# Optimization experiments

Measured on AMD Instinct MI355X. Metric: run time of the kernel, lower is better.

Reference implementation:

```python
import jax, jax.numpy as jnp
import numpy as np

N, E, F, EF, D, G = 25000, 100000, 32, 8, 64, 1000


def setup_inputs() -> dict:
    key = jax.random.key(0)
    ks = jax.random.split(key, 32)
    p = lambda k, shape: (jax.random.normal(k, shape, jnp.float32) * 0.05)
    inp = {
        "x": jax.random.normal(ks[0], (N, F), jnp.float32),
        "edge_index": jax.random.randint(ks[1], (2, E), 0, N, jnp.int64 if jax.config.jax_enable_x64 else jnp.int32),
        "edge_attr": jax.random.uniform(ks[2], (E, EF), jnp.float32),
        "batch": jnp.sort(jax.random.randint(ks[3], (N,), 0, G, jnp.int32)),
        # lin0
        "W0": p(ks[4], (F, D)), "b0": p(ks[5], (D,)),
        # edge MLP: Linear(EF, D) -> ReLU -> Linear(D, D*D)
        "We1": p(ks[6], (EF, D)), "be1": p(ks[7], (D,)),
        "We2": p(ks[8], (D, D * D)), "be2": p(ks[9], (D * D,)),
        # NNConv root weight + bias
        "Wroot": p(ks[10], (D, D)), "bconv": p(ks[11], (D,)),
        # GRU (single layer): gate order r, z, n
        "Wi": p(ks[12], (3 * D, D)), "Wh": p(ks[13], (3 * D, D)),
        "bi": p(ks[14], (3 * D,)), "bh": p(ks[15], (3 * D,)),
        # heads
        "W11": p(ks[16], (D, D)), "b11": p(ks[17], (D,)),
        "W12": p(ks[18], (D, D)), "b12": p(ks[19], (D,)),
        "W13": p(ks[20], (D, 1)), "b13": p(ks[21], (1,)),
        "W21": p(ks[22], (D, D)), "b21": p(ks[23], (D,)),
        "W22": p(ks[24], (D, D)), "b22": p(ks[25], (D,)),
        "W23": p(ks[26], (D, 1)), "b23": p(ks[27], (1,)),
    }
    return inp


def reference(x, edge_index, edge_attr, batch,
              W0, b0, We1, be1, We2, be2, Wroot, bconv,
              Wi, Wh, bi, bh,
              W11, b11, W12, b12, W13, b13,
              W21, b21, W22, b22, W23, b23):
    src, dst = edge_index[0], edge_index[1]
    # lin0 + relu
    x1 = jax.nn.relu(x @ W0 + b0)                      # [N, D]
    h = x1                                              # GRU hidden init
    # NNConv: dynamic per-edge weight via edge MLP
    ew = (jax.nn.relu(edge_attr @ We1 + be1) @ We2 + be2).reshape(E, D, D)
    msg = jnp.einsum('ei,eio->eo', x1[src], ew)        # per-edge matmul
    agg = jax.ops.segment_sum(msg, dst, num_segments=N)
    x2 = jax.nn.relu(x1 @ Wroot + agg + bconv)         # [N, D]
    # GRU single step (torch gate order: r, z, n)
    gi = x2 @ Wi.T + bi
    gh = h @ Wh.T + bh
    r = jax.nn.sigmoid(gi[:, :D] + gh[:, :D])
    z = jax.nn.sigmoid(gi[:, D:2 * D] + gh[:, D:2 * D])
    n = jnp.tanh(gi[:, 2 * D:] + r * gh[:, 2 * D:])
    hn = (1.0 - z) * n + z * h                          # [N, D]
    # graph pooling (scatter_add over batch)
    pooled = jax.ops.segment_sum(hn, batch, num_segments=G)  # [G, D]
    # two MLP heads
    x_1 = jax.nn.relu(pooled @ W11 + b11)
    x_1 = jax.nn.relu(x_1 @ W12 + b12)
    x_1 = x_1 @ W13 + b13
    x_2 = jax.nn.relu(pooled @ W21 + b21)
    x_2 = jax.nn.relu(x_2 @ W22 + b22)
    x_2 = x_2 @ W23 + b23
    return jnp.concatenate([x_1, x_2], axis=1)          # [G, 2]
```

## Files before the change

kernel.cpp:

```cpp
#include <hip/hip_runtime.h>
#include <hip/hip_bf16.h>
#include <hip/hip_fp16.h>

#define NN 25000
#define NE 100000
#define FIN 32
#define DD 64
#define NG 1000

typedef unsigned short u16;
typedef __attribute__((ext_vector_type(8))) short short8;
typedef __attribute__((ext_vector_type(8))) _Float16 f16x8;
typedef __attribute__((ext_vector_type(4))) float f32x4;

__device__ __forceinline__ u16 f2h(float f) {
    __half h = __float2half(f);
    return __builtin_bit_cast(u16, h);
}
__device__ __forceinline__ float h2f(u16 u) {
    __half h = __builtin_bit_cast(__half, u);
    return __half2float(h);
}
__device__ __forceinline__ f16x8 s2h(short8 v) { return __builtin_bit_cast(f16x8, v); }
__device__ __forceinline__ bool idx_is_i64(const int* e) {
    return (e[1] == 0) & (e[3] == 0) & (e[5] == 0) & (e[7] == 0) & (e[9] == 0);
}
__device__ __forceinline__ int ld_src(const int* e, int i, bool i64) {
    return i64 ? e[2 * i] : e[i];
}
__device__ __forceinline__ int ld_dst(const int* e, int i, bool i64) {
    return i64 ? e[2 * (NE + i)] : e[NE + i];
}

__global__ __launch_bounds__(256) void k_pre(const float* __restrict__ x,
                                             const float* __restrict__ W0,
                                             const float* __restrict__ b0,
                                             u16* __restrict__ x1b,
                                             const float* __restrict__ We2,
                                             const float* __restrict__ be2,
                                             float* __restrict__ agg,
                                             float* __restrict__ pooled,
                                             u16* __restrict__ Bt2,
                                             const float* __restrict__ Wi,
                                             const float* __restrict__ Wh,
                                             const float* __restrict__ Wroot,
                                             u16* __restrict__ Wib,
                                             u16* __restrict__ Whb,
                                             u16* __restrict__ Wrb) {
    __shared__ float sbuf[4096 + 512];
    int tid = threadIdx.x;
    if (blockIdx.x < 1563) {
        float* sW = sbuf;
        float* sx = sbuf + 4096;
        for (int i = tid; i < FIN * DD; i += 256) sW[i] = W0[i];
        int nbase = blockIdx.x * 16;
        for (int i = tid; i < 16 * FIN; i += 256) {
            int nl = i >> 5, f = i & 31;
            int n = nbase + nl;
            sx[i] = (n < NN) ? x[n * FIN + f] : 0.f;
        }
        __syncthreads();
        int lane = tid & 63, nl = tid >> 6;
        float bias = b0[lane];
        #pragma unroll
        for (int rr = 0; rr < 4; rr++) {
            int row = nl * 4 + rr;
            int n = nbase + row;
            if (n < NN) {
                float acc = bias;
                #pragma unroll
                for (int f = 0; f < FIN; f++) acc += sx[row * FIN + f] * sW[f * DD + lane];
                x1b[n * DD + lane] = f2h(fmaxf(acc, 0.f));
            }
        }
    } else if (blockIdx.x < 1628) {
        int kc = blockIdx.x - 1563;
        const float* src = (kc < 64) ? (We2 + kc * 4096) : be2;
        for (int i = tid; i < 4096; i += 256) sbuf[i] = src[i];
        __syncthreads();
        for (int m = tid; m < 4096; m += 256) {
            int f = m >> 9, ln = (m >> 3) & 63, j = m & 7;
            int s = f >> 2, c = f & 3;
            int o = c * 16 + (ln & 15);
            int rlow = s * 32 + (ln >> 4) * 8 + j;
            Bt2[kc * 4096 + m] = f2h(sbuf[rlow * 64 + o]);
        }
    } else {
        int tid0 = (blockIdx.x - 1628) * 256 + threadIdx.x;
        const int STR = 256 * 256;
        for (int i = tid0; i < NN * DD; i += STR) agg[i] = 0.f;
        for (int i = tid0; i < NG * DD; i += STR) pooled[i] = 0.f;
        for (int i = tid0; i < 12288; i += STR) {
            int fr = i >> 9, lane = (i >> 3) & 63, j = i & 7;
            int c = fr >> 1, kcx = fr & 1;
            int row = c * 16 + (lane & 15);
            int col = kcx * 32 + (lane >> 4) * 8 + j;
            Wib[i] = f2h(Wi[row * 64 + col]);
            Whb[i] = f2h(Wh[row * 64 + col]);
        }
        for (int i = tid0; i < 4096; i += STR) {
            int fr = i >> 9, lane = (i >> 3) & 63, j = i & 7;
            int c = fr >> 1, kcx = fr & 1;
            int row = c * 16 + (lane & 15);
            int col = kcx * 32 + (lane >> 4) * 8 + j;
            Wrb[i] = f2h(Wroot[col * 64 + row]);
        }
    }
}

__global__ __launch_bounds__(512, 4) void k_msg(const float* __restrict__ ea,
                                                const int* __restrict__ eidx,
                                                const float* __restrict__ We1,
                                                const float* __restrict__ be1,
                                                const u16* __restrict__ x1b,
                                                const u16* __restrict__ Bt2,
                                                float* __restrict__ agg) {
    __shared__ __align__(16) u16 sX[128 * 72];
    __shared__ __align__(16) u16 sTh[65 * 128 + 64];
    __shared__ float sWe1[8 * 64];
    __shared__ float sbe1[64];
    __shared__ int sDst[128];
    const int tid = threadIdx.x;
    const int lane = tid & 63, wv = tid >> 6;
    const int ll = lane & 15, quad = lane >> 4;
    const int rh = wv >> 2, cq = wv & 3;
    const int e0 = blockIdx.x * 128;
    const bool i64 = idx_is_i64(eidx);

    if (tid < 512) sWe1[tid] = We1[tid];
    if (tid < 64) sbe1[tid] = be1[tid];
    if (tid < 128) {
        sDst[tid] = (e0 + tid < NE) ? ld_dst(eidx, e0 + tid, i64) : 0;
        sTh[64 * 128 + tid] = 0x3C00;
    }

    const int el4 = tid >> 2, seg = tid & 3;
    const int eg4 = e0 + el4;
    {
        if (eg4 < NE) {
            int sv = ld_src(eidx, eg4, i64);
            const u16* xr = x1b + sv * 64 + seg * 16;
            *(uint4*)&sX[el4 * 72 + seg * 16]     = *(const uint4*)(xr);
            *(uint4*)&sX[el4 * 72 + seg * 16 + 8] = *(const uint4*)(xr + 8);
        } else {
            uint4 z = make_uint4(0, 0, 0, 0);
            *(uint4*)&sX[el4 * 72 + seg * 16]     = z;
            *(uint4*)&sX[el4 * 72 + seg * 16 + 8] = z;
        }
    }
    float eav[8];
    if (eg4 < NE) {
        f32x4 v0 = *(const f32x4*)(ea + eg4 * 8);
        f32x4 v1 = *(const f32x4*)(ea + eg4 * 8 + 4);
        #pragma unroll
        for (int f = 0; f < 4; f++) { eav[f] = v0[f]; eav[4 + f] = v1[f]; }
    } else {
        #pragma unroll
        for (int f = 0; f < 8; f++) eav[f] = 0.f;
    }
    __syncthreads();

    {
        int k0 = seg * 16;
        for (int kk = 0; kk < 16; kk++) {
            int k = k0 + kk;
            float acc = sbe1[k];
            #pragma unroll
            for (int f = 0; f < 8; f++) acc += eav[f] * sWe1[f * 64 + k];
            sTh[k * 128 + el4] = f2h((eg4 < NE) ? fmaxf(acc, 0.f) : 0.f);
        }
    }
    __syncthreads();

    short8 xa[4][2];
    #pragma unroll
    for (int rt = 0; rt < 4; rt++)
        #pragma unroll
        for (int s = 0; s < 2; s++)
            xa[rt][s] = *(const short8*)&sX[(rh * 64 + rt * 16 + ll) * 72 + s * 32 + quad * 8];

    f32x4 msg[4];
    #pragma unroll
    for (int rt = 0; rt < 4; rt++) msg[rt] = (f32x4){0.f, 0.f, 0.f, 0.f};

    const u16* gB0 = Bt2 + (0 * 4 + cq) * 512 + lane * 8;
    const u16* gB1 = Bt2 + (1 * 4 + cq) * 512 + lane * 8;
    const f32x4 zero = (f32x4){0.f, 0.f, 0.f, 0.f};
    const int tkoff = rh * 64 + quad * 4;

    #define LDR(dst, kcv, rtv) dst = *(const uint2*)&sTh[(kcv) * 128 + tkoff + (rtv) * 16];
    #define CVT(t, raw)                                                      \
        {                                                                    \
            __half2 _a = __builtin_bit_cast(__half2, (raw).x);               \
            __half2 _b = __builtin_bit_cast(__half2, (raw).y);               \
            float2 _fa = __half22float2(_a);                                 \
            float2 _fb = __half22float2(_b);                                 \
            t = (f32x4){_fa.x, _fa.y, _fb.x, _fb.y};                         \
        }

    short8 c00 = *(const short8*)(gB0);
    short8 c01 = *(const short8*)(gB1);
    short8 c10 = *(const short8*)(gB0 + 4096);
    short8 c11 = *(const short8*)(gB1 + 4096);
    uint2 tkA[4], tkB[4];
    #pragma unroll
    for (int rt = 0; rt < 4; rt++) LDR(tkA[rt], 0, rt);

    for (int kc = 0; kc < 62; kc += 2) {
        short8 n00 = *(const short8*)(gB0 + (kc + 2) * 4096);
        short8 n01 = *(const short8*)(gB1 + (kc + 2) * 4096);
        short8 n10 = *(const short8*)(gB0 + (kc + 3) * 4096);
        short8 n11 = *(const short8*)(gB1 + (kc + 3) * 4096);
        #pragma unroll
        for (int rt = 0; rt < 4; rt++) LDR(tkB[rt], kc + 1, rt);
        #pragma unroll
        for (int rt = 0; rt < 4; rt++) {
            f32x4 q0 = __builtin_amdgcn_mfma_f32_16x16x32_f16(s2h(xa[rt][0]), s2h(c00), zero, 0, 0, 0);
            f32x4 q1 = __builtin_amdgcn_mfma_f32_16x16x32_f16(s2h(xa[rt][1]), s2h(c01), zero, 0, 0, 0);
            f32x4 t; CVT(t, tkA[rt]);
            msg[rt] += t * q0;
            msg[rt] += t * q1;
        }
        #pragma unroll
        for (int rt = 0; rt < 4; rt++) LDR(tkA[rt], kc + 2, rt);
        #pragma unroll
        for (int rt = 0; rt < 4; rt++) {
            f32x4 q0 = __builtin_amdgcn_mfma_f32_16x16x32_f16(s2h(xa[rt][0]), s2h(c10), zero, 0, 0, 0);
            f32x4 q1 = __builtin_amdgcn_mfma_f32_16x16x32_f16(s2h(xa[rt][1]), s2h(c11), zero, 0, 0, 0);
            f32x4 t; CVT(t, tkB[rt]);
            msg[rt] += t * q0;
            msg[rt] += t * q1;
        }
        c00 = n00; c01 = n01; c10 = n10; c11 = n11;
    }
    {
        short8 n00 = *(const short8*)(gB0 + 64 * 4096);
        short8 n01 = *(const short8*)(gB1 + 64 * 4096);
        #pragma unroll
        for (int rt = 0; rt < 4; rt++) LDR(tkB[rt], 63, rt);
        #pragma unroll
        for (int rt = 0; rt < 4; rt++) {
            f32x4 q0 = __builtin_amdgcn_mfma_f32_16x16x32_f16(s2h(xa[rt][0]), s2h(c00), zero, 0, 0, 0);
            f32x4 q1 = __builtin_amdgcn_mfma_f32_16x16x32_f16(s2h(xa[rt][1]), s2h(c01), zero, 0, 0, 0);
            f32x4 t; CVT(t, tkA[rt]);
            msg[rt] += t * q0;
            msg[rt] += t * q1;
        }
        #pragma unroll
        for (int rt = 0; rt < 4; rt++) LDR(tkA[rt], 64, rt);
        #pragma unroll
        for (int rt = 0; rt < 4; rt++) {
            f32x4 q0 = __builtin_amdgcn_mfma_f32_16x16x32_f16(s2h(xa[rt][0]), s2h(c10), zero, 0, 0, 0);
            f32x4 q1 = __builtin_amdgcn_mfma_f32_16x16x32_f16(s2h(xa[rt][1]), s2h(c11), zero, 0, 0, 0);
            f32x4 t; CVT(t, tkB[rt]);
            msg[rt] += t * q0;
            msg[rt] += t * q1;
        }
        #pragma unroll
        for (int rt = 0; rt < 4; rt++) {
            f32x4 q0 = __builtin_amdgcn_mfma_f32_16x16x32_f16(s2h(xa[rt][0]), s2h(n00), zero, 0, 0, 0);
            f32x4 q1 = __builtin_amdgcn_mfma_f32_16x16x32_f16(s2h(xa[rt][1]), s2h(n01), zero, 0, 0, 0);
            f32x4 t; CVT(t, tkA[rt]);
            msg[rt] += t * q0;
            msg[rt] += t * q1;
        }
    }
    #undef LDR
    #undef CVT

    #pragma unroll
    for (int rt = 0; rt < 4; rt++) {
        #pragma unroll
        for (int r = 0; r < 4; r++) {
            int el = rh * 64 + rt * 16 + quad * 4 + r;
            int eg = e0 + el;
            if (eg < NE) {
                int d = sDst[el];
                atomicAdd(&agg[d * 64 + cq * 16 + ll], msg[rt][r]);
            }
        }
    }
}

__global__ __launch_bounds__(256) void k_gru(const u16* __restrict__ x1b,
                                             const float* __restrict__ agg,
                                             const u16* __restrict__ Wib,
                                             const u16* __restrict__ Whb,
                                             const u16* __restrict__ Wrb,
                                             const float* __restrict__ bconv,
                                             const float* __restrict__ bi,
                                             const float* __restrict__ bh,
                                             const int* __restrict__ batch,
                                             float* __restrict__ pooled) {
    __shared__ __align__(16) u16 sX2[64 * 72];
    __shared__ float hbuf[64 * 65];
    __shared__ int sBatch[64];
    const int tid = threadIdx.x;
    const int lane = tid & 63, wv = tid >> 6;
    const int ll = lane & 15, quad = lane >> 4;
    const int n0 = blockIdx.x * 64;

    if (tid < 64) {
        int n = n0 + tid;
        sBatch[tid] = (n < NN) ? batch[n] : -1;
    }

    short8 ha[2];
    {
        int n = n0 + wv * 16 + ll;
        #pragma unroll
        for (int kc = 0; kc < 2; kc++) {
            if (n < NN) ha[kc] = *(const short8*)(x1b + n * 64 + kc * 32 + quad * 8);
            else        ha[kc] = (short8){0,0,0,0,0,0,0,0};
        }
    }
    f32x4 acc1[4];
    #pragma unroll
    for (int c = 0; c < 4; c++) acc1[c] = (f32x4){0.f, 0.f, 0.f, 0.f};
    #pragma unroll
    for (int kc = 0; kc < 2; kc++) {
        #pragma unroll
        for (int c = 0; c < 4; c++) {
            short8 b = *(const short8*)&Wrb[(c * 2 + kc) * 512 + lane * 8];
            acc1[c] = __builtin_amdgcn_mfma_f32_16x16x32_f16(s2h(ha[kc]), s2h(b), acc1[c], 0, 0, 0);
        }
    }
    #pragma unroll
    for (int c = 0; c < 4; c++) {
        int col = c * 16 + ll;
        float bcv = bconv[col];
        #pragma unroll
        for (int r = 0; r < 4; r++) {
            int row = wv * 16 + quad * 4 + r;
            int n = n0 + row;
            float v = 0.f;
            if (n < NN) v = fmaxf(acc1[c][r] + agg[n * 64 + col] + bcv, 0.f);
            sX2[row * 72 + col] = f2h(v);
        }
    }
    __syncthreads();

    short8 xa[2];
    #pragma unroll
    for (int kc = 0; kc < 2; kc++)
        xa[kc] = *(const short8*)&sX2[(wv * 16 + ll) * 72 + kc * 32 + quad * 8];

    f32x4 agi[12], agh[12];
    #pragma unroll
    for (int c = 0; c < 12; c++) { agi[c] = (f32x4){0.f,0.f,0.f,0.f}; agh[c] = (f32x4){0.f,0.f,0.f,0.f}; }
    #pragma unroll
    for (int kc = 0; kc < 2; kc++) {
        #pragma unroll
        for (int c = 0; c < 12; c++) {
            short8 bi8 = *(const short8*)&Wib[(c * 2 + kc) * 512 + lane * 8];
            short8 bh8 = *(const short8*)&Whb[(c * 2 + kc) * 512 + lane * 8];
            agi[c] = __builtin_amdgcn_mfma_f32_16x16x32_f16(s2h(xa[kc]), s2h(bi8), agi[c], 0, 0, 0);
            agh[c] = __builtin_amdgcn_mfma_f32_16x16x32_f16(s2h(ha[kc]), s2h(bh8), agh[c], 0, 0, 0);
        }
    }

    float hnv[4][4];
    #pragma unroll
    for (int c0 = 0; c0 < 4; c0++) {
        int d = c0 * 16 + ll;
        float bir = bi[d],        bhr = bh[d];
        float biz = bi[64 + d],   bhz = bh[64 + d];
        float bin = bi[128 + d],  bhn = bh[128 + d];
        #pragma unroll
        for (int r = 0; r < 4; r++) {
            int row = wv * 16 + quad * 4 + r;
            int n = n0 + row;
            float gir = agi[c0][r] + bir,     ghr = agh[c0][r] + bhr;
            float giz = agi[c0 + 4][r] + biz, ghz = agh[c0 + 4][r] + bhz;
            float gin = agi[c0 + 8][r] + bin, ghn = agh[c0 + 8][r] + bhn;
            float rg = 1.f / (1.f + __expf(-(gir + ghr)));
            float zg = 1.f / (1.f + __expf(-(giz + ghz)));
            float ng = tanhf(gin + rg * ghn);
            float hv = (n < NN) ? h2f(x1b[n * 64 + d]) : 0.f;
            hnv[c0][r] = (n < NN) ? ((1.f - zg) * ng + zg * hv) : 0.f;
        }
    }
    __syncthreads();

    #pragma unroll
    for (int c0 = 0; c0 < 4; c0++) {
        int d = c0 * 16 + ll;
        #pragma unroll
        for (int r = 0; r < 4; r++) {
            int row = wv * 16 + quad * 4 + r;
            hbuf[row * 65 + d] = hnv[c0][r];
        }
    }
    __syncthreads();

    {
        int d = lane;
        float sum = 0.f;
        int pb = sBatch[wv * 16];
        #pragma unroll
        for (int rr = 0; rr < 16; rr++) {
            int row = wv * 16 + rr;
            int b = sBatch[row];
            float v = hbuf[row * 65 + d];
            if (b != pb) {
                if (pb >= 0) atomicAdd(&pooled[pb * 64 + d], sum);
                sum = v; pb = b;
            } else {
                sum += v;
            }
        }
        if (pb >= 0) atomicAdd(&pooled[pb * 64 + d], sum);
    }
}

__global__ __launch_bounds__(256) void k_heads(const float* __restrict__ pooled,
                                               const float* __restrict__ W11, const float* __restrict__ b11,
                                               const float* __restrict__ W12, const float* __restrict__ b12,
                                               const float* __restrict__ W13, const float* __restrict__ b13,
                                               const float* __restrict__ W21, const float* __restrict__ b21,
                                               const float* __restrict__ W22, const float* __restrict__ b22,
                                               const float* __restrict__ W23, const float* __restrict__ b23,
                                               float* __restrict__ out) {
    __shared__ float sV[4][64];
    __shared__ float sA[4][64];
    int tid = threadIdx.x, lane = tid & 63, wv = tid >> 6;
    int g = blockIdx.x * 4 + wv;
    if (g >= NG) return;
    float p = pooled[g * 64 + lane];
    sV[wv][lane] = p;
    float y[2];
    const float* W1s[2] = {W11, W21}; const float* b1s[2] = {b11, b21};
    const float* W2s[2] = {W12, W22}; const float* b2s[2] = {b12, b22};
    const float* W3s[2] = {W13, W23}; const float* b3s[2] = {b13, b23};
    #pragma unroll
    for (int hd = 0; hd < 2; hd++) {
        float a = b1s[hd][lane];
        #pragma unroll 8
        for (int i = 0; i < 64; i++) a += sV[wv][i] * W1s[hd][i * 64 + lane];
        a = fmaxf(a, 0.f);
        sA[wv][lane] = a;
        float a2 = b2s[hd][lane];
        #pragma unroll 8
        for (int i = 0; i < 64; i++) a2 += sA[wv][i] * W2s[hd][i * 64 + lane];
        a2 = fmaxf(a2, 0.f);
        float part = a2 * W3s[hd][lane];
        #pragma unroll
        for (int m = 32; m > 0; m >>= 1) part += __shfl_xor(part, m, 64);
        y[hd] = part + b3s[hd][0];
    }
    if (lane == 0) {
        out[g * 2 + 0] = y[0];
        out[g * 2 + 1] = y[1];
    }
}

extern "C" void kernel_launch(void* const* d_in, const int* in_sizes, int n_in,
                              void* d_out, int out_size, void* d_ws, size_t ws_size,
                              hipStream_t stream) {
    const float* x     = (const float*)d_in[0];
    const int* eidx    = (const int*)d_in[1];
    const float* ea    = (const float*)d_in[2];
    const int* batch   = (const int*)d_in[3];
    const float* W0    = (const float*)d_in[4];  const float* b0    = (const float*)d_in[5];
    const float* We1   = (const float*)d_in[6];  const float* be1   = (const float*)d_in[7];
    const float* We2   = (const float*)d_in[8];  const float* be2   = (const float*)d_in[9];
    const float* Wroot = (const float*)d_in[10]; const float* bconv = (const float*)d_in[11];
    const float* Wi    = (const float*)d_in[12]; const float* Wh    = (const float*)d_in[13];
    const float* bi    = (const float*)d_in[14]; const float* bh    = (const float*)d_in[15];
    const float* W11   = (const float*)d_in[16]; const float* b11   = (const float*)d_in[17];
    const float* W12   = (const float*)d_in[18]; const float* b12   = (const float*)d_in[19];
    const float* W13   = (const float*)d_in[20]; const float* b13   = (const float*)d_in[21];
    const float* W21   = (const float*)d_in[22]; const float* b21   = (const float*)d_in[23];
    const float* W22   = (const float*)d_in[24]; const float* b22   = (const float*)d_in[25];
    const float* W23   = (const float*)d_in[26]; const float* b23   = (const float*)d_in[27];
    float* out = (float*)d_out;

    char* ws = (char*)d_ws;
    float* agg    = (float*)(ws);
    u16*   x1b    = (u16*)(ws + 6400000);
    u16*   Bt2    = (u16*)(ws + 9600000);
    float* pooled = (float*)(ws + 10132480);
    u16*   Wib    = (u16*)(ws + 10388480);
    u16*   Whb    = (u16*)(ws + 10413056);
    u16*   Wrb    = (u16*)(ws + 10437632);

    hipLaunchKernelGGL(k_pre, dim3(1884), dim3(256), 0, stream,
                       x, W0, b0, x1b, We2, be2, agg, pooled, Bt2,
                       Wi, Wh, Wroot, Wib, Whb, Wrb);
    hipLaunchKernelGGL(k_msg, dim3(782), dim3(512), 0, stream, ea, eidx, We1, be1, x1b, Bt2, agg);
    hipLaunchKernelGGL(k_gru, dim3(391), dim3(256), 0, stream, x1b, agg,
                       Wib, Whb, Wrb, bconv, bi, bh, batch, pooled);
    hipLaunchKernelGGL(k_heads, dim3(250), dim3(256), 0, stream, pooled,
                       W11, b11, W12, b12, W13, b13, W21, b21, W22, b22, W23, b23, out);
}
```

Before: 226.2 us.

## Run MLP heads on MFMA with fp16 pre-packed weights; faster GRU activations

The per-graph MLP heads are rewritten to process 64 graphs per block with 16x16x32 fp16 MFMA instructions. The head weights are pre-converted to fp16 in the MFMA fragment layout inside the preprocessing kernel. The GRU gate math swaps tanhf and the plain divides for __expf and __fdividef forms. This cuts the scalar FMA work and the launch grid for the heads kernel, at the cost of fp16 precision in the heads and a less accurate tanh.

```diff
diff --git a/kernel.cpp b/kernel.cpp
--- a/kernel.cpp
+++ b/kernel.cpp
@@ -46,7 +46,15 @@
                                              const float* __restrict__ Wroot,
                                              u16* __restrict__ Wib,
                                              u16* __restrict__ Whb,
-                                             u16* __restrict__ Wrb) {
+                                             u16* __restrict__ Wrb,
+                                             const float* __restrict__ W11,
+                                             const float* __restrict__ W12,
+                                             const float* __restrict__ W21,
+                                             const float* __restrict__ W22,
+                                             u16* __restrict__ W11b,
+                                             u16* __restrict__ W12b,
+                                             u16* __restrict__ W21b,
+                                             u16* __restrict__ W22b) {
     __shared__ float sbuf[4096 + 512];
     int tid = threadIdx.x;
     if (blockIdx.x < 1563) {
@@ -103,7 +111,12 @@
             int c = fr >> 1, kcx = fr & 1;
             int row = c * 16 + (lane & 15);
             int col = kcx * 32 + (lane >> 4) * 8 + j;
-            Wrb[i] = f2h(Wroot[col * 64 + row]);
+            int idx = col * 64 + row;
+            Wrb[i]  = f2h(Wroot[idx]);
+            W11b[i] = f2h(W11[idx]);
+            W12b[i] = f2h(W12[idx]);
+            W21b[i] = f2h(W21[idx]);
+            W22b[i] = f2h(W22[idx]);
         }
     }
 }
@@ -373,9 +386,11 @@
             float gir = agi[c0][r] + bir,     ghr = agh[c0][r] + bhr;
             float giz = agi[c0 + 4][r] + biz, ghz = agh[c0 + 4][r] + bhz;
             float gin = agi[c0 + 8][r] + bin, ghn = agh[c0 + 8][r] + bhn;
-            float rg = 1.f / (1.f + __expf(-(gir + ghr)));
-            float zg = 1.f / (1.f + __expf(-(giz + ghz)));
-            float ng = tanhf(gin + rg * ghn);
+            float rg = __fdividef(1.f, 1.f + __expf(-(gir + ghr)));
+            float zg = __fdividef(1.f, 1.f + __expf(-(giz + ghz)));
+            float xt = gin + rg * ghn;
+            float e2 = __expf(2.f * xt);
+            float ng = 1.f - __fdividef(2.f, e2 + 1.f);
             float hv = (n < NN) ? h2f(x1b[n * 64 + d]) : 0.f;
             hnv[c0][r] = (n < NN) ? ((1.f - zg) * ng + zg * hv) : 0.f;
         }
@@ -414,43 +429,101 @@
 }
 
 __global__ __launch_bounds__(256) void k_heads(const float* __restrict__ pooled,
-                                               const float* __restrict__ W11, const float* __restrict__ b11,
-                                               const float* __restrict__ W12, const float* __restrict__ b12,
+                                               const u16* __restrict__ W11b, const float* __restrict__ b11,
+                                               const u16* __restrict__ W12b, const float* __restrict__ b12,
                                                const float* __restrict__ W13, const float* __restrict__ b13,
-                                               const float* __restrict__ W21, const float* __restrict__ b21,
-                                               const float* __restrict__ W22, const float* __restrict__ b22,
+                                               const u16* __restrict__ W21b, const float* __restrict__ b21,
+                                               const u16* __restrict__ W22b, const float* __restrict__ b22,
                                                const float* __restrict__ W23, const float* __restrict__ b23,
                                                float* __restrict__ out) {
-    __shared__ float sV[4][64];
-    __shared__ float sA[4][64];
-    int tid = threadIdx.x, lane = tid & 63, wv = tid >> 6;
-    int g = blockIdx.x * 4 + wv;
-    if (g >= NG) return;
-    float p = pooled[g * 64 + lane];
-    sV[wv][lane] = p;
-    float y[2];
-    const float* W1s[2] = {W11, W21}; const float* b1s[2] = {b11, b21};
-    const float* W2s[2] = {W12, W22}; const float* b2s[2] = {b12, b22};
+    __shared__ __align__(16) u16 sY[64 * 72];
+    const int tid = threadIdx.x;
+    const int lane = tid & 63, wv = tid >> 6;
+    const int ll = lane & 15, quad = lane >> 4;
+    const int g0 = blockIdx.x * 64;
+    const f32x4 zero = (f32x4){0.f, 0.f, 0.f, 0.f};
+
+    short8 pa[2];
+    {
+        int g = g0 + wv * 16 + ll;
+        #pragma unroll
+        for (int kc = 0; kc < 2; kc++) {
+            if (g < NG) {
+                const float* pr = pooled + g * 64 + kc * 32 + quad * 8;
+                f32x4 v0 = *(const f32x4*)(pr);
+                f32x4 v1 = *(const f32x4*)(pr + 4);
+                short8 s;
+                #pragma unroll
+                for (int j = 0; j < 4; j++) {
+                    s[j]     = (short)f2h(v0[j]);
+                    s[4 + j] = (short)f2h(v1[j]);
+                }
+                pa[kc] = s;
+            } else {
+                pa[kc] = (short8){0,0,0,0,0,0,0,0};
+            }
+        }
+    }
+
+    const u16* W1s[2] = {W11b, W21b}; const float* b1s[2] = {b11, b21};
+    const u16* W2s[2] = {W12b, W22b}; const float* b2s[2] = {b12, b22};
     const float* W3s[2] = {W13, W23}; const float* b3s[2] = {b13, b23};
+
     #pragma unroll
     for (int hd = 0; hd < 2; hd++) {
-        float a = b1s[hd][lane];
-        #pragma unroll 8
-        for (int i = 0; i < 64; i++) a += sV[wv][i] * W1s[hd][i * 64 + lane];
-        a = fmaxf(a, 0.f);
-        sA[wv][lane] = a;
-        float a2 = b2s[hd][lane];
-        #pragma unroll 8
-        for (int i = 0; i < 64; i++) a2 += sA[wv][i] * W2s[hd][i * 64 + lane];
-        a2 = fmaxf(a2, 0.f);
-        float part = a2 * W3s[hd][lane];
-        #pragma unroll
-        for (int m = 32; m > 0; m >>= 1) part += __shfl_xor(part, m, 64);
-        y[hd] = part + b3s[hd][0];
-    }
-    if (lane == 0) {
-        out[g * 2 + 0] = y[0];
-        out[g * 2 + 1] = y[1];
+        f32x4 a1[4];
+        #pragma unroll
+        for (int c = 0; c < 4; c++) a1[c] = zero;
+        #pragma unroll
+        for (int kc = 0; kc < 2; kc++)
+            #pragma unroll
+            for (int c = 0; c < 4; c++) {
+                short8 b = *(const short8*)&W1s[hd][(c * 2 + kc) * 512 + lane * 8];
+                a1[c] = __builtin_amdgcn_mfma_f32_16x16x32_f16(s2h(pa[kc]), s2h(b), a1[c], 0, 0, 0);
+            }
+        #pragma unroll
+        for (int c = 0; c < 4; c++) {
+            int col = c * 16 + ll;
+            float bv = b1s[hd][col];
+            #pragma unroll
+            for (int r = 0; r < 4; r++) {
+                int row = wv * 16 + quad * 4 + r;
+                sY[row * 72 + col] = f2h(fmaxf(a1[c][r] + bv, 0.f));
+            }
+        }
+        __syncthreads();
+        short8 ya[2];
+        #pragma unroll
+        for (int kc = 0; kc < 2; kc++)
+            ya[kc] = *(const short8*)&sY[(wv * 16 + ll) * 72 + kc * 32 + quad * 8];
+        f32x4 a2[4];
+        #pragma unroll
+        for (int c = 0; c < 4; c++) a2[c] = zero;
+        #pragma unroll
+        for (int kc = 0; kc < 2; kc++)
+            #pragma unroll
+            for (int c = 0; c < 4; c++) {
+                short8 b = *(const short8*)&W2s[hd][(c * 2 + kc) * 512 + lane * 8];
+                a2[c] = __builtin_amdgcn_mfma_f32_16x16x32_f16(s2h(ya[kc]), s2h(b), a2[c], 0, 0, 0);
+            }
+        #pragma unroll
+        for (int r = 0; r < 4; r++) {
+            float part = 0.f;
+            #pragma unroll
+            for (int c = 0; c < 4; c++) {
+                int col = c * 16 + ll;
+                part += fmaxf(a2[c][r] + b2s[hd][col], 0.f) * W3s[hd][col];
+            }
+            part += __shfl_xor(part, 1, 64);
+            part += __shfl_xor(part, 2, 64);
+            part += __shfl_xor(part, 4, 64);
+            part += __shfl_xor(part, 8, 64);
+            if (ll == 0) {
+                int g = g0 + wv * 16 + quad * 4 + r;
+                if (g < NG) out[g * 2 + hd] = part + b3s[hd][0];
+            }
+        }
+        __syncthreads();
     }
 }
 
@@ -483,13 +556,18 @@
     u16*   Wib    = (u16*)(ws + 10388480);
     u16*   Whb    = (u16*)(ws + 10413056);
     u16*   Wrb    = (u16*)(ws + 10437632);
+    u16*   W11b   = (u16*)(ws + 10445824);
+    u16*   W12b   = (u16*)(ws + 10454016);
+    u16*   W21b   = (u16*)(ws + 10462208);
+    u16*   W22b   = (u16*)(ws + 10470400);
 
     hipLaunchKernelGGL(k_pre, dim3(1884), dim3(256), 0, stream,
                        x, W0, b0, x1b, We2, be2, agg, pooled, Bt2,
-                       Wi, Wh, Wroot, Wib, Whb, Wrb);
+                       Wi, Wh, Wroot, Wib, Whb, Wrb,
+                       W11, W12, W21, W22, W11b, W12b, W21b, W22b);
     hipLaunchKernelGGL(k_msg, dim3(782), dim3(512), 0, stream, ea, eidx, We1, be1, x1b, Bt2, agg);
     hipLaunchKernelGGL(k_gru, dim3(391), dim3(256), 0, stream, x1b, agg,
                        Wib, Whb, Wrb, bconv, bi, bh, batch, pooled);
-    hipLaunchKernelGGL(k_heads, dim3(250), dim3(256), 0, stream, pooled,
-                       W11, b11, W12, b12, W13, b13, W21, b21, W22, b22, W23, b23, out);
-}
+    hipLaunchKernelGGL(k_heads, dim3(16), dim3(256), 0, stream, pooled,
+                       W11b, b11, W12b, b12, W13, b13, W21b, b21, W22b, b22, W23, b23, out);
+}
```

Measured after the change: 224.1 us (median of 2 runs). About the same (-0.9%).
